# Kernel optimization log

Hardware: AMD Instinct MI355X
Metric: run time of the kernel (lower is better)

## Reference

```python
import jax, jax.numpy as jnp
import numpy as np

ENT_SIZE = 100000; REL_SIZE = 500; ENT_DIM = 256; REL_DIM = 256; H = 256
E = 2048; S = 32; N = 1024; THRESHOLD = 1.0; EPS = 1e-5


def _xav(k, shape):
    fan_in = shape[-1]
    fan_out = shape[-2] if len(shape) > 1 else shape[-1]
    std = (2.0 / (fan_in + fan_out)) ** 0.5
    return jax.random.normal(k, shape, jnp.float32) * std


def setup_inputs() -> dict:
    key = jax.random.key(0)
    ks = jax.random.split(key, 16)
    inp = {}
    inp["neighbors"] = jax.random.randint(ks[0], (E, S), 0, ENT_SIZE)
    inp["pos_h"] = jax.random.randint(ks[1], (N,), 0, E)
    inp["pos_t"] = jax.random.randint(ks[2], (N,), 0, E)
    inp["pos_r"] = jax.random.randint(ks[3], (N,), 0, REL_SIZE)
    inp["neg_h"] = jax.random.randint(ks[4], (N,), 0, E)
    inp["neg_t"] = jax.random.randint(ks[5], (N,), 0, E)
    inp["neg_r"] = jax.random.randint(ks[6], (N,), 0, REL_SIZE)
    inp["ent_embed"] = _xav(ks[7], (ENT_SIZE + 1, ENT_DIM))
    inp["rel_embed"] = _xav(ks[8], (REL_SIZE, REL_DIM))
    inp["trans"] = _xav(ks[9], (2 * REL_SIZE, REL_DIM, ENT_DIM))
    inp["W_ih_f"] = _xav(ks[10], (4 * H, ENT_DIM)); inp["W_hh_f"] = _xav(ks[11], (4 * H, H))
    inp["W_ih_b"] = _xav(ks[12], (4 * H, ENT_DIM)); inp["W_hh_b"] = _xav(ks[13], (4 * H, H))
    inp["b_f"] = jnp.zeros((4 * H,), jnp.float32)
    inp["b_b"] = jnp.zeros((4 * H,), jnp.float32)
    inp["W_lin"] = _xav(ks[14], (ENT_DIM, 2 * H)); inp["b_lin"] = jnp.zeros((ENT_DIM,), jnp.float32)
    inp["gamma"] = jnp.ones((ENT_DIM,), jnp.float32); inp["beta"] = jnp.zeros((ENT_DIM,), jnp.float32)
    return inp


def _lstm_final(x, W_ih, W_hh, b):
    # x: [E,S,D] -> final hidden state [E,H] (PyTorch LSTM gate order i,f,g,o; b = b_ih+b_hh)
    h0 = jnp.zeros((x.shape[0], H), x.dtype)
    def step(carry, xt):
        h, c = carry
        g = xt @ W_ih.T + h @ W_hh.T + b  # [E,4H]
        i, f, gg, o = jnp.split(g, 4, axis=-1)
        c = jax.nn.sigmoid(f) * c + jax.nn.sigmoid(i) * jnp.tanh(gg)
        h = jax.nn.sigmoid(o) * jnp.tanh(c)
        return (h, c), None
    (h, _), _ = jax.lax.scan(step, (h0, h0), jnp.swapaxes(x, 0, 1))
    return h


def _context(ent_embed, neighbors, W_ih_f, W_hh_f, b_f, W_ih_b, W_hh_b, b_b, W_lin, b_lin, gamma, beta):
    x_seq = ent_embed[neighbors]  # [E,S,D]
    h_f = _lstm_final(x_seq, W_ih_f, W_hh_f, b_f)
    h_b = _lstm_final(x_seq[:, ::-1], W_ih_b, W_hh_b, b_b)
    lin = jnp.concatenate([h_f, h_b], -1) @ W_lin.T + b_lin  # [E,ENT_DIM]
    # BatchNorm1d in training mode: batch stats (biased variance)
    mu = lin.mean(0)
    var = lin.var(0)
    return jnp.tanh(gamma * (lin - mu) * jax.lax.rsqrt(var + EPS) + beta)


def _score(trans, rel_embed, ctx, h_idx, r_idx, t_idx):
    Wh = trans[r_idx]             # [N,REL_DIM,ENT_DIM] (grouped expert GEMV, batched)
    Wt = trans[r_idx + REL_SIZE]
    d = jnp.einsum('nre,ne->nr', Wh, ctx[h_idx]) - jnp.einsum('nre,ne->nr', Wt, ctx[t_idx])
    return jnp.linalg.norm(d + rel_embed[r_idx], axis=1)


def reference(neighbors, pos_h, pos_t, pos_r, neg_h, neg_t, neg_r,
              ent_embed, rel_embed, trans, W_ih_f, W_hh_f, W_ih_b, W_hh_b,
              b_f, b_b, W_lin, b_lin, gamma, beta):
    ctx = _context(ent_embed, neighbors, W_ih_f, W_hh_f, b_f, W_ih_b, W_hh_b, b_b,
                   W_lin, b_lin, gamma, beta)
    pos_n = _score(trans, rel_embed, ctx, pos_h, pos_r, pos_t)
    neg_n = _score(trans, rel_embed, ctx, neg_h, neg_r, neg_t)
    return jnp.sum(pos_n + jax.nn.relu(THRESHOLD - neg_n))
```

## Files before the change

### kernel.cpp

```cpp
#include <hip/hip_runtime.h>

constexpr int kE   = 2048;
constexpr int kS   = 32;
constexpr int kD   = 256;
constexpr int kK   = 512;
constexpr int kREL = 500;
constexpr int kN   = 1024;

typedef unsigned short u16;
typedef __attribute__((ext_vector_type(8))) _Float16 f16x8;
typedef __attribute__((ext_vector_type(4))) float    f32x4;
typedef __attribute__((ext_vector_type(4))) unsigned short us4;

static __device__ __forceinline__ u16 f2h(float f) {
  _Float16 h = (_Float16)f;
  return __builtin_bit_cast(u16, h);
}
static __device__ __forceinline__ float h2f(u16 v) {
  _Float16 h = __builtin_bit_cast(_Float16, v);
  return (float)h;
}
static __device__ __forceinline__ float sigf(float x) { return 1.f / (1.f + __expf(-x)); }
static __device__ __forceinline__ float tanhfast(float x) {
  float e = __expf(2.f * x);
  return 1.f - 2.f / (e + 1.f);
}
static __device__ __forceinline__ void gl_lds16(const void* g, void* l) {
  __builtin_amdgcn_global_load_lds((const __attribute__((address_space(1))) unsigned int*)g,
                                   (__attribute__((address_space(3))) unsigned int*)l, 16, 0, 0);
}

__global__ void prep_weights(const float* __restrict__ Wih_f, const float* __restrict__ Whh_f,
                             const float* __restrict__ Wih_b, const float* __restrict__ Whh_b,
                             const float* __restrict__ Wlin_in,
                             u16* __restrict__ Wv3, u16* __restrict__ Whhr,
                             u16* __restrict__ Wlin) {
  int idx = blockIdx.x * 256 + threadIdx.x;
  if (idx < 65536) {
    int q  = idx & 2047;
    int ch = (idx >> 11) & 3;
    int y  = (idx >> 13) & 3;
    int d  = idx >> 15;
    int j  = q >> 3;
    int k8 = (q & 7) ^ (j & 7);
    int jg = y * 256 + j;
    int g = (jg >> 4) & 3, u = (jg >> 6) * 16 + (jg & 15);
    int R = g * 256 + u;
    int k = ch * 64 + k8 * 8;
    const float* src = (d ? Wih_b : Wih_f) + R * 256 + k;
    ushort oa[8];
#pragma unroll
    for (int i = 0; i < 8; i++) oa[i] = f2h(src[i]);
    *(uint4*)((char*)Wv3 + (size_t)idx * 16) = *(uint4*)oa;
  } else if (idx < 131072) {
    int i2 = idx - 65536;
    int d = i2 >> 15;
    int j = (i2 & 32767) >> 5;
    int k = (i2 & 31) * 8;
    int g = (j >> 4) & 3, u = (j >> 6) * 16 + (j & 15);
    int R = g * 256 + u;
    const float* src = (d ? Whh_b : Whh_f) + R * 256 + k;
    ushort oa[8];
#pragma unroll
    for (int i = 0; i < 8; i++) oa[i] = f2h(src[i]);
    *(uint4*)((char*)Whhr + (size_t)i2 * 16) = *(uint4*)oa;
  } else if (idx < 131072 + 16384) {
    int q = (idx - 131072) * 8;
#pragma unroll
    for (int i = 0; i < 8; i++) Wlin[q + i] = f2h(Wlin_in[q + i]);
  }
}

__global__ void gather_x(const int* __restrict__ neighbors, const float* __restrict__ ent,
                         u16* __restrict__ ximg) {
  int idx = blockIdx.x * 256 + threadIdx.x;
  int q    = idx & 511;
  int ch   = (idx >> 9) & 3;
  int tile = (idx >> 11) & 31;
  int s    = idx >> 16;
  int row = q >> 3;
  int c8 = (q & 7) ^ (row & 7);
  int e = tile * 64 + row;
  int k = ch * 64 + c8 * 8;
  int nb = neighbors[e * 32 + s];
  const float* src = ent + (size_t)nb * 256 + k;
  float4 v0 = *(const float4*)src;
  float4 v1 = *(const float4*)(src + 4);
  ushort oa[8];
  oa[0] = f2h(v0.x); oa[1] = f2h(v0.y); oa[2] = f2h(v0.z); oa[3] = f2h(v0.w);
  oa[4] = f2h(v1.x); oa[5] = f2h(v1.y); oa[6] = f2h(v1.z); oa[7] = f2h(v1.w);
  *(uint4*)((char*)ximg + (size_t)idx * 16) = *(uint4*)oa;
}

__global__ __launch_bounds__(256) void xgemm(
    const u16* __restrict__ ximg, const u16* __restrict__ Wv3,
    const float* __restrict__ b_f, const float* __restrict__ b_b,
    u16* __restrict__ gx, int t0, int T) {
  __shared__ __align__(16) char As[8192];
  __shared__ __align__(16) char Bs[32768];
  const int tid = threadIdx.x, lane = tid & 63, w = tid >> 6;
  const int l15 = lane & 15, lq = lane >> 4;
  const int row0 = blockIdx.x * 64;
  const int y = blockIdx.y, dir = blockIdx.z;
  const int tt = row0 >> 11;
  const int e0 = row0 & 2047;
  const int etile = e0 >> 6;
  const int s = dir ? (31 - (t0 + tt)) : (t0 + tt);
  const char* imgA = (const char*)ximg + (size_t)(s * 32 + etile) * 32768;
  const char* imgB = (const char*)Wv3 + (size_t)(dir * 4 + y) * 131072;
  const float* bd = dir ? b_b : b_f;
  const int u = (y * 4 + w) * 16 + l15;

  f32x4 acc[4][4];
#pragma unroll
  for (int n = 0; n < 4; n++) {
    float bv = bd[n * 256 + u];
#pragma unroll
    for (int m = 0; m < 4; m++) acc[m][n] = (f32x4){bv, bv, bv, bv};
  }

  for (int ch = 0; ch < 4; ++ch) {
#pragma unroll
    for (int i = 0; i < 2; i++)
      gl_lds16(imgA + ch * 8192 + i * 4096 + w * 1024 + lane * 16,
               As + i * 4096 + w * 1024);
#pragma unroll
    for (int i = 0; i < 8; i++)
      gl_lds16(imgB + (size_t)ch * 32768 + i * 4096 + w * 1024 + lane * 16,
               Bs + i * 4096 + w * 1024);
    __syncthreads();
#pragma unroll
    for (int ks = 0; ks < 2; ++ks) {
      const int kb = ks * 64 + lq * 16;
      f16x8 a[4], b[4];
#pragma unroll
      for (int m = 0; m < 4; m++) {
        int row = m * 16 + l15;
        a[m] = *(const f16x8*)(As + row * 128 + (kb ^ ((row & 7) << 4)));
      }
#pragma unroll
      for (int n = 0; n < 4; n++) {
        int row = w * 64 + n * 16 + l15;
        b[n] = *(const f16x8*)(Bs + row * 128 + (kb ^ ((row & 7) << 4)));
      }
#pragma unroll
      for (int m = 0; m < 4; m++)
#pragma unroll
        for (int n = 0; n < 4; n++)
          acc[m][n] = __builtin_amdgcn_mfma_f32_16x16x32_f16(a[m], b[n], acc[m][n], 0, 0, 0);
    }
    __syncthreads();
  }

  u16* out = gx + (((size_t)dir * T + tt) * kE) * 1024;
#pragma unroll
  for (int m = 0; m < 4; m++)
#pragma unroll
    for (int r = 0; r < 4; r++) {
      int e = e0 + m * 16 + lq * 4 + r;
      us4 o;
      o[0] = f2h(acc[m][0][r]); o[1] = f2h(acc[m][1][r]);
      o[2] = f2h(acc[m][2][r]); o[3] = f2h(acc[m][3][r]);
      __builtin_nontemporal_store(o, (us4*)(out + ((size_t)e * 256 + u) * 4));
    }
}

__global__ __launch_bounds__(256) void lstm_step(
    const u16* __restrict__ gx, const u16* __restrict__ Whhr,
    const u16* __restrict__ hprev, u16* __restrict__ hnext,
    float* __restrict__ cbuf, int tt, int T) {
  const int tid = threadIdx.x, lane = tid & 63, w = tid >> 6;
  const int l15 = lane & 15, lq = lane >> 4;
  const int bid = blockIdx.x;
  const int dir = bid >> 8;
  const int rem = bid & 255;
  const int jg = rem >> 6;
  const int et = rem & 63;
  const int e0 = et * 32;
  const int c0 = jg * 256 + w * 64;
  const int unit = (c0 >> 6) * 16 + l15;

  const u16* Wd  = Whhr + ((size_t)dir * 1024 + c0) * kD;
  const u16* hpd = hprev + (size_t)dir * kE * kD;
  u16* hnd = hnext + (size_t)dir * kE * kD;
  float* cd = cbuf + (size_t)dir * kE * kD;
  const u16* gp = gx + ((size_t)dir * T + tt) * kE * 1024;

  f32x4 acc[2][4];
#pragma unroll
  for (int m = 0; m < 2; m++)
#pragma unroll
    for (int r = 0; r < 4; r++) {
      us4 g = __builtin_nontemporal_load(
          (const us4*)(gp + (size_t)(e0 + m * 16 + lq * 4 + r) * 1024 + unit * 4));
#pragma unroll
      for (int n = 0; n < 4; n++) acc[m][n][r] = h2f(g[n]);
    }

  const int klane = lq * 8;
#pragma unroll
  for (int ks = 0; ks < 8; ks++) {
    const int ka = ks * 32 + klane;
    f16x8 a[2], b[4];
#pragma unroll
    for (int m = 0; m < 2; m++)
      a[m] = *(const f16x8*)(hpd + (size_t)(e0 + m * 16 + l15) * kD + ka);
#pragma unroll
    for (int n = 0; n < 4; n++)
      b[n] = *(const f16x8*)(Wd + (size_t)(n * 16 + l15) * kD + ka);
#pragma unroll
    for (int m = 0; m < 2; m++)
#pragma unroll
      for (int n = 0; n < 4; n++)
        acc[m][n] = __builtin_amdgcn_mfma_f32_16x16x32_f16(a[m], b[n], acc[m][n], 0, 0, 0);
  }

#pragma unroll
  for (int m = 0; m < 2; m++)
#pragma unroll
    for (int r = 0; r < 4; r++) {
      int row = e0 + m * 16 + lq * 4 + r;
      size_t off = (size_t)row * kD + unit;
      float gi = acc[m][0][r];
      float gf = acc[m][1][r];
      float gg = acc[m][2][r];
      float go = acc[m][3][r];
      float c_old = cd[off];
      float cn = sigf(gf) * c_old + sigf(gi) * tanhfast(gg);
      cd[off] = cn;
      hnd[off] = f2h(sigf(go) * tanhfast(cn));
    }
}

static __device__ __forceinline__ void gemm_tile(
    const u16* __restrict__ Alo, const u16* __restrict__ Ahi,
    const u16* __restrict__ W, int e0,
    u16* As, u16* Bs, f32x4 (&acc)[4][4]) {
  const int tid = threadIdx.x;
  const int lane = tid & 63;
  const int w = tid >> 6;
#pragma unroll
  for (int m = 0; m < 4; m++)
#pragma unroll
    for (int n = 0; n < 4; n++) acc[m][n] = (f32x4){0.f, 0.f, 0.f, 0.f};

  for (int ch = 0; ch < 8; ++ch) {
    const int k0 = ch * 64;
    __syncthreads();
    const u16* Asrc = (k0 < 256) ? Alo : Ahi;
    const int kbase = (k0 < 256) ? k0 : (k0 - 256);
#pragma unroll
    for (int i = 0; i < 2; i++) {
      int idx = tid + i * 256;
      int row = idx >> 3, c8 = idx & 7;
      uint4 v = *(const uint4*)(Asrc + (size_t)(e0 + row) * 256 + kbase + c8 * 8);
      *(uint4*)((char*)As + row * 128 + ((c8 * 16) ^ ((row & 7) << 4))) = v;
    }
#pragma unroll
    for (int i = 0; i < 8; i++) {
      int idx = tid + i * 256;
      int j = idx >> 3, c8 = idx & 7;
      uint4 v = *(const uint4*)(W + (size_t)j * kK + k0 + c8 * 8);
      *(uint4*)((char*)Bs + j * 128 + ((c8 * 16) ^ ((j & 7) << 4))) = v;
    }
    __syncthreads();
#pragma unroll
    for (int ks = 0; ks < 2; ++ks) {
      const int kb = ks * 64 + (lane >> 4) * 16;
      f16x8 a[4], b[4];
#pragma unroll
      for (int m = 0; m < 4; m++) {
        int row = m * 16 + (lane & 15);
        a[m] = *(const f16x8*)((const char*)As + row * 128 + (kb ^ ((row & 7) << 4)));
      }
#pragma unroll
      for (int n = 0; n < 4; n++) {
        int row = w * 64 + n * 16 + (lane & 15);
        b[n] = *(const f16x8*)((const char*)Bs + row * 128 + (kb ^ ((row & 7) << 4)));
      }
#pragma unroll
      for (int m = 0; m < 4; m++)
#pragma unroll
        for (int n = 0; n < 4; n++)
          acc[m][n] = __builtin_amdgcn_mfma_f32_16x16x32_f16(a[m], b[n], acc[m][n], 0, 0, 0);
    }
  }
}

__global__ __launch_bounds__(256) void lin_kernel(
    const u16* __restrict__ hf, const u16* __restrict__ hb,
    const u16* __restrict__ Wl, const float* __restrict__ b_lin,
    float* __restrict__ lin) {
  __shared__ __align__(16) char smem[40960];
  u16* As = (u16*)smem;
  u16* Bs = (u16*)(smem + 8192);
  const int tid = threadIdx.x, lane = tid & 63, w = tid >> 6;
  const int e0 = blockIdx.x * 64;
  f32x4 acc[4][4];
  gemm_tile(hf, hb, Wl, e0, As, Bs, acc);
#pragma unroll
  for (int m = 0; m < 4; m++)
#pragma unroll
    for (int n = 0; n < 4; n++)
#pragma unroll
      for (int r = 0; r < 4; r++) {
        int e = e0 + m * 16 + (lane >> 4) * 4 + r;
        int col = w * 64 + n * 16 + (lane & 15);
        lin[(size_t)e * 256 + col] = acc[m][n][r] + b_lin[col];
      }
}

__global__ void bn_stats(const float* __restrict__ lin, float* __restrict__ part) {
  int b = blockIdx.x, c = threadIdx.x;
  float s = 0.f, s2 = 0.f;
  for (int e = b * 32; e < b * 32 + 32; ++e) {
    float x = lin[(size_t)e * 256 + c];
    s += x; s2 += x * x;
  }
  part[b * 256 + c] = s;
  part[64 * 256 + b * 256 + c] = s2;
}

__global__ void bn_apply(const float* __restrict__ lin, const float* __restrict__ part,
                         const float* __restrict__ gamma, const float* __restrict__ beta,
                         float* __restrict__ ctx) {
  int c = threadIdx.x;
  float s = 0.f, s2 = 0.f;
  for (int b = 0; b < 64; b++) { s += part[b * 256 + c]; s2 += part[64 * 256 + b * 256 + c]; }
  float mu = s * (1.f / 2048.f);
  float rsig = rsqrtf(s2 * (1.f / 2048.f) - mu * mu + 1e-5f);
  float ga = gamma[c], be = beta[c];
  int e0 = blockIdx.x * 8;
  for (int e = e0; e < e0 + 8; ++e) {
    float x = lin[(size_t)e * 256 + c];
    ctx[(size_t)e * 256 + c] = tanhf(ga * (x - mu) * rsig + be);
  }
}

__global__ void group_rel(const int* __restrict__ pr, const int* __restrict__ nr,
                          int* __restrict__ offs, int* __restrict__ list) {
  __shared__ int cnt[512], sc[512], cur[512];
  int tid = threadIdx.x;
  cnt[tid] = 0;
  __syncthreads();
  for (int i = tid; i < 2 * kN; i += 512) {
    int r = (i < kN) ? pr[i] : nr[i - kN];
    atomicAdd(&cnt[r], 1);
  }
  __syncthreads();
  sc[tid] = cnt[tid];
  __syncthreads();
  for (int d = 1; d < 512; d <<= 1) {
    int v = (tid >= d) ? sc[tid - d] : 0;
    __syncthreads();
    sc[tid] += v;
    __syncthreads();
  }
  int excl = (tid == 0) ? 0 : sc[tid - 1];
  cur[tid] = excl;
  if (tid <= kREL) offs[tid] = excl;
  __syncthreads();
  for (int i = tid; i < 2 * kN; i += 512) {
    int r = (i < kN) ? pr[i] : nr[i - kN];
    int p = atomicAdd(&cur[r], 1);
    list[p] = i;
  }
}

__global__ __launch_bounds__(256) void score_grouped(
    const float* __restrict__ ctx, const float* __restrict__ trans,
    const float* __restrict__ rel_embed,
    const int* __restrict__ ph, const int* __restrict__ pt,
    const int* __restrict__ nh, const int* __restrict__ nt,
    const int* __restrict__ offs, const int* __restrict__ list,
    float* __restrict__ scores) {
  int r = blockIdx.x;
  int start = offs[r], end = offs[r + 1];
  if (start >= end) return;
  int tid = threadIdx.x;
  __shared__ float cs[8][2][256];
  __shared__ float red[8][4];
  float relv = rel_embed[r * 256 + tid];
  const float4* Whp = (const float4*)(trans + (size_t)r * 65536 + (size_t)tid * 256);
  const float4* Wtp = (const float4*)(trans + ((size_t)r + kREL) * 65536 + (size_t)tid * 256);

  for (int chunk = start; chunk < end; chunk += 8) {
    int G = min(8, end - chunk);
    for (int j = 0; j < G; j++) {
      int i = list[chunk + j];
      int hh = (i < kN) ? ph[i] : nh[i - kN];
      int tt = (i < kN) ? pt[i] : nt[i - kN];
      cs[j][0][tid] = ctx[(size_t)hh * 256 + tid];
      cs[j][1][tid] = ctx[(size_t)tt * 256 + tid];
    }
    __syncthreads();
    float acc[8];
#pragma unroll
    for (int j = 0; j < 8; j++) acc[j] = relv;
#pragma unroll 2
    for (int q = 0; q < 64; q++) {
      float4 w1 = Whp[q];
      float4 w2 = Wtp[q];
#pragma unroll
      for (int j = 0; j < 8; j++) {
        float4 xh = *(const float4*)&cs[j][0][q * 4];
        float4 xt = *(const float4*)&cs[j][1][q * 4];
        acc[j] += w1.x * xh.x + w1.y * xh.y + w1.z * xh.z + w1.w * xh.w
                - (w2.x * xt.x + w2.y * xt.y + w2.z * xt.z + w2.w * xt.w);
      }
    }
    for (int j = 0; j < G; j++) {
      float sq = acc[j] * acc[j];
      for (int o = 32; o; o >>= 1) sq += __shfl_down(sq, o);
      if ((tid & 63) == 0) red[j][tid >> 6] = sq;
    }
    __syncthreads();
    if (tid < G) {
      float s = red[tid][0] + red[tid][1] + red[tid][2] + red[tid][3];
      scores[list[chunk + tid]] = sqrtf(s);
    }
    __syncthreads();
  }
}

__global__ void final_reduce(const float* __restrict__ scores, float* __restrict__ out) {
  int tid = threadIdx.x;
  float a = 0.f;
  for (int i = tid; i < 2 * kN; i += 256) {
    float s = scores[i];
    a += (i < kN) ? s : fmaxf(0.f, 1.f - s);
  }
  for (int off = 32; off; off >>= 1) a += __shfl_down(a, off);
  __shared__ float w4[4];
  if ((tid & 63) == 0) w4[tid >> 6] = a;
  __syncthreads();
  if (tid == 0) out[0] = w4[0] + w4[1] + w4[2] + w4[3];
}

extern "C" void kernel_launch(void* const* d_in, const int* in_sizes, int n_in,
                              void* d_out, int out_size, void* d_ws, size_t ws_size,
                              hipStream_t stream) {
  const int*   neighbors = (const int*)d_in[0];
  const int*   pos_h = (const int*)d_in[1];
  const int*   pos_t = (const int*)d_in[2];
  const int*   pos_r = (const int*)d_in[3];
  const int*   neg_h = (const int*)d_in[4];
  const int*   neg_t = (const int*)d_in[5];
  const int*   neg_r = (const int*)d_in[6];
  const float* ent_embed = (const float*)d_in[7];
  const float* rel_embed = (const float*)d_in[8];
  const float* trans = (const float*)d_in[9];
  const float* W_ih_f = (const float*)d_in[10];
  const float* W_hh_f = (const float*)d_in[11];
  const float* W_ih_b = (const float*)d_in[12];
  const float* W_hh_b = (const float*)d_in[13];
  const float* b_f = (const float*)d_in[14];
  const float* b_b = (const float*)d_in[15];
  const float* W_lin = (const float*)d_in[16];
  const float* b_lin = (const float*)d_in[17];
  const float* gamma = (const float*)d_in[18];
  const float* beta = (const float*)d_in[19];

  char* ws = (char*)d_ws;
  size_t off = 0;
  auto alloc = [&](size_t bytes) {
    void* p = ws + off;
    off = (off + bytes + 255) & ~(size_t)255;
    return p;
  };
  u16* Wv3    = (u16*)alloc((size_t)65536 * 16);
  u16* Whhr   = (u16*)alloc((size_t)2 * 1024 * kD * 2);
  u16* Wlin   = (u16*)alloc((size_t)256 * kK * 2);
  u16* ximg   = (u16*)alloc((size_t)2097152 * 16);
  u16* h0     = (u16*)alloc((size_t)2 * kE * kD * 2);
  u16* h1     = (u16*)alloc((size_t)2 * kE * kD * 2);
  float* cbuf = (float*)alloc((size_t)2 * kE * kD * 4);
  float* lin  = (float*)alloc((size_t)kE * 256 * 4);
  float* part = (float*)alloc((size_t)2 * 64 * 256 * 4);
  float* ctx  = (float*)alloc((size_t)kE * 256 * 4);
  float* scores = (float*)alloc((size_t)2 * kN * 4);
  int* offsb  = (int*)alloc((size_t)512 * 4);
  int* list   = (int*)alloc((size_t)2 * kN * 4);
  size_t fixed_end = off;
  (void)in_sizes; (void)n_in; (void)out_size;

  int T = 2;
  for (int cand = 32; cand >= 2; cand >>= 1) {
    size_t gxb = (size_t)2 * cand * kE * 1024 * 2;
    if (fixed_end + gxb + (1 << 20) <= ws_size) { T = cand; break; }
  }
  u16* gx = (u16*)alloc((size_t)2 * T * kE * 1024 * 2);

  hipMemsetAsync(h0, 0, (size_t)2 * kE * kD * 2, stream);
  hipMemsetAsync(cbuf, 0, (size_t)2 * kE * kD * 4, stream);

  prep_weights<<<576, 256, 0, stream>>>(W_ih_f, W_hh_f, W_ih_b, W_hh_b, W_lin,
                                        Wv3, Whhr, Wlin);
  gather_x<<<8192, 256, 0, stream>>>(neighbors, ent_embed, ximg);
  group_rel<<<1, 512, 0, stream>>>(pos_r, neg_r, offsb, list);

  for (int t0 = 0; t0 < kS; t0 += T) {
    xgemm<<<dim3(T * 32, 4, 2), 256, 0, stream>>>(ximg, Wv3, b_f, b_b, gx, t0, T);
    for (int tt = 0; tt < T; tt++) {
      int t = t0 + tt;
      const u16* hp = (t & 1) ? h1 : h0;
      u16* hn = (t & 1) ? h0 : h1;
      lstm_step<<<512, 256, 0, stream>>>(gx, Whhr, hp, hn, cbuf, tt, T);
    }
  }

  lin_kernel<<<32, 256, 0, stream>>>(h0, h0 + (size_t)kE * kD, Wlin, b_lin, lin);
  bn_stats<<<64, 256, 0, stream>>>(lin, part);
  bn_apply<<<256, 256, 0, stream>>>(lin, part, gamma, beta, ctx);
  score_grouped<<<kREL, 256, 0, stream>>>(ctx, trans, rel_embed,
                                          pos_h, pos_t, neg_h, neg_t, offsb, list, scores);
  final_reduce<<<1, 256, 0, stream>>>(scores, (float*)d_out);
}
```

Before: 831.4 us.

## Fuse next-step input GEMM into recurrent step kernel with double-buffered gates

Each LSTM step now runs in a single kernel. The first 512 blocks do the recurrent update for step t, and the extra 256 blocks compute the input projection for step t+1 into a ping-pong gate buffer. This replaces the large batched xgemm over many timesteps with per-step overlap and shrinks the gate buffer so it can stay cache-resident, which is why the nontemporal hints are dropped. It also fuses prep_weights with gather_x, and folds the BN partial statistics into lin_kernel to remove bn_stats. The cost is more launches of a heavier kernel, LDS allocated even for recurrent blocks (possibly lowering occupancy), and a shorter xgemm that is less efficient per launch.

```diff
diff --git a/kernel.cpp b/kernel.cpp
--- a/kernel.cpp
+++ b/kernel.cpp
@@ -30,82 +30,77 @@
                                    (__attribute__((address_space(3))) unsigned int*)l, 16, 0, 0);
 }
 
-__global__ void prep_weights(const float* __restrict__ Wih_f, const float* __restrict__ Whh_f,
-                             const float* __restrict__ Wih_b, const float* __restrict__ Whh_b,
-                             const float* __restrict__ Wlin_in,
-                             u16* __restrict__ Wv3, u16* __restrict__ Whhr,
-                             u16* __restrict__ Wlin) {
-  int idx = blockIdx.x * 256 + threadIdx.x;
-  if (idx < 65536) {
-    int q  = idx & 2047;
-    int ch = (idx >> 11) & 3;
-    int y  = (idx >> 13) & 3;
-    int d  = idx >> 15;
-    int j  = q >> 3;
-    int k8 = (q & 7) ^ (j & 7);
-    int jg = y * 256 + j;
-    int g = (jg >> 4) & 3, u = (jg >> 6) * 16 + (jg & 15);
-    int R = g * 256 + u;
-    int k = ch * 64 + k8 * 8;
-    const float* src = (d ? Wih_b : Wih_f) + R * 256 + k;
+__global__ void prep_gather(const float* __restrict__ Wih_f, const float* __restrict__ Whh_f,
+                            const float* __restrict__ Wih_b, const float* __restrict__ Whh_b,
+                            const float* __restrict__ Wlin_in,
+                            const int* __restrict__ neighbors, const float* __restrict__ ent,
+                            u16* __restrict__ Wv3, u16* __restrict__ Whhr,
+                            u16* __restrict__ Wlin, u16* __restrict__ ximg) {
+  if (blockIdx.x < 576) {
+    int idx = blockIdx.x * 256 + threadIdx.x;
+    if (idx < 65536) {
+      int q  = idx & 2047;
+      int ch = (idx >> 11) & 3;
+      int y  = (idx >> 13) & 3;
+      int d  = idx >> 15;
+      int j  = q >> 3;
+      int k8 = (q & 7) ^ (j & 7);
+      int jg = y * 256 + j;
+      int g = (jg >> 4) & 3, u = (jg >> 6) * 16 + (jg & 15);
+      int R = g * 256 + u;
+      int k = ch * 64 + k8 * 8;
+      const float* src = (d ? Wih_b : Wih_f) + R * 256 + k;
+      ushort oa[8];
+#pragma unroll
+      for (int i = 0; i < 8; i++) oa[i] = f2h(src[i]);
+      *(uint4*)((char*)Wv3 + (size_t)idx * 16) = *(uint4*)oa;
+    } else if (idx < 131072) {
+      int i2 = idx - 65536;
+      int d = i2 >> 15;
+      int j = (i2 & 32767) >> 5;
+      int k = (i2 & 31) * 8;
+      int g = (j >> 4) & 3, u = (j >> 6) * 16 + (j & 15);
+      int R = g * 256 + u;
+      const float* src = (d ? Whh_b : Whh_f) + R * 256 + k;
+      ushort oa[8];
+#pragma unroll
+      for (int i = 0; i < 8; i++) oa[i] = f2h(src[i]);
+      *(uint4*)((char*)Whhr + (size_t)i2 * 16) = *(uint4*)oa;
+    } else if (idx < 131072 + 16384) {
+      int q = (idx - 131072) * 8;
+#pragma unroll
+      for (int i = 0; i < 8; i++) Wlin[q + i] = f2h(Wlin_in[q + i]);
+    }
+  } else {
+    int idx = (blockIdx.x - 576) * 256 + threadIdx.x;
+    int q    = idx & 511;
+    int ch   = (idx >> 9) & 3;
+    int tile = (idx >> 11) & 31;
+    int s    = idx >> 16;
+    int row = q >> 3;
+    int c8 = (q & 7) ^ (row & 7);
+    int e = tile * 64 + row;
+    int k = ch * 64 + c8 * 8;
+    int nb = neighbors[e * 32 + s];
+    const float* src = ent + (size_t)nb * 256 + k;
+    float4 v0 = *(const float4*)src;
+    float4 v1 = *(const float4*)(src + 4);
     ushort oa[8];
-#pragma unroll
-    for (int i = 0; i < 8; i++) oa[i] = f2h(src[i]);
-    *(uint4*)((char*)Wv3 + (size_t)idx * 16) = *(uint4*)oa;
-  } else if (idx < 131072) {
-    int i2 = idx - 65536;
-    int d = i2 >> 15;
-    int j = (i2 & 32767) >> 5;
-    int k = (i2 & 31) * 8;
-    int g = (j >> 4) & 3, u = (j >> 6) * 16 + (j & 15);
-    int R = g * 256 + u;
-    const float* src = (d ? Whh_b : Whh_f) + R * 256 + k;
-    ushort oa[8];
-#pragma unroll
-    for (int i = 0; i < 8; i++) oa[i] = f2h(src[i]);
-    *(uint4*)((char*)Whhr + (size_t)i2 * 16) = *(uint4*)oa;
-  } else if (idx < 131072 + 16384) {
-    int q = (idx - 131072) * 8;
-#pragma unroll
-    for (int i = 0; i < 8; i++) Wlin[q + i] = f2h(Wlin_in[q + i]);
-  }
-}
-
-__global__ void gather_x(const int* __restrict__ neighbors, const float* __restrict__ ent,
-                         u16* __restrict__ ximg) {
-  int idx = blockIdx.x * 256 + threadIdx.x;
-  int q    = idx & 511;
-  int ch   = (idx >> 9) & 3;
-  int tile = (idx >> 11) & 31;
-  int s    = idx >> 16;
-  int row = q >> 3;
-  int c8 = (q & 7) ^ (row & 7);
-  int e = tile * 64 + row;
-  int k = ch * 64 + c8 * 8;
-  int nb = neighbors[e * 32 + s];
-  const float* src = ent + (size_t)nb * 256 + k;
-  float4 v0 = *(const float4*)src;
-  float4 v1 = *(const float4*)(src + 4);
-  ushort oa[8];
-  oa[0] = f2h(v0.x); oa[1] = f2h(v0.y); oa[2] = f2h(v0.z); oa[3] = f2h(v0.w);
-  oa[4] = f2h(v1.x); oa[5] = f2h(v1.y); oa[6] = f2h(v1.z); oa[7] = f2h(v1.w);
-  *(uint4*)((char*)ximg + (size_t)idx * 16) = *(uint4*)oa;
-}
-
-__global__ __launch_bounds__(256) void xgemm(
+    oa[0] = f2h(v0.x); oa[1] = f2h(v0.y); oa[2] = f2h(v0.z); oa[3] = f2h(v0.w);
+    oa[4] = f2h(v1.x); oa[5] = f2h(v1.y); oa[6] = f2h(v1.z); oa[7] = f2h(v1.w);
+    *(uint4*)((char*)ximg + (size_t)idx * 16) = *(uint4*)oa;
+  }
+}
+
+static __device__ __forceinline__ void xgemm_body(
     const u16* __restrict__ ximg, const u16* __restrict__ Wv3,
     const float* __restrict__ b_f, const float* __restrict__ b_b,
-    u16* __restrict__ gx, int t0, int T) {
-  __shared__ __align__(16) char As[8192];
-  __shared__ __align__(16) char Bs[32768];
+    u16* __restrict__ gx, int ts, int etile, int y, int dir,
+    char* As, char* Bs) {
   const int tid = threadIdx.x, lane = tid & 63, w = tid >> 6;
   const int l15 = lane & 15, lq = lane >> 4;
-  const int row0 = blockIdx.x * 64;
-  const int y = blockIdx.y, dir = blockIdx.z;
-  const int tt = row0 >> 11;
-  const int e0 = row0 & 2047;
-  const int etile = e0 >> 6;
-  const int s = dir ? (31 - (t0 + tt)) : (t0 + tt);
+  const int e0 = etile * 64;
+  const int s = dir ? (31 - ts) : ts;
   const char* imgA = (const char*)ximg + (size_t)(s * 32 + etile) * 32768;
   const char* imgB = (const char*)Wv3 + (size_t)(dir * 4 + y) * 131072;
   const float* bd = dir ? b_b : b_f;
@@ -152,7 +147,7 @@
     __syncthreads();
   }
 
-  u16* out = gx + (((size_t)dir * T + tt) * kE) * 1024;
+  u16* out = gx + ((size_t)(dir * 2 + (ts & 1)) * kE) * 1024;
 #pragma unroll
   for (int m = 0; m < 4; m++)
 #pragma unroll
@@ -161,17 +156,16 @@
       us4 o;
       o[0] = f2h(acc[m][0][r]); o[1] = f2h(acc[m][1][r]);
       o[2] = f2h(acc[m][2][r]); o[3] = f2h(acc[m][3][r]);
-      __builtin_nontemporal_store(o, (us4*)(out + ((size_t)e * 256 + u) * 4));
-    }
-}
-
-__global__ __launch_bounds__(256) void lstm_step(
+      *(us4*)(out + ((size_t)e * 256 + u) * 4) = o;
+    }
+}
+
+static __device__ __forceinline__ void rec_body(
     const u16* __restrict__ gx, const u16* __restrict__ Whhr,
     const u16* __restrict__ hprev, u16* __restrict__ hnext,
-    float* __restrict__ cbuf, int tt, int T) {
+    float* __restrict__ cbuf, int t, int bid) {
   const int tid = threadIdx.x, lane = tid & 63, w = tid >> 6;
   const int l15 = lane & 15, lq = lane >> 4;
-  const int bid = blockIdx.x;
   const int dir = bid >> 8;
   const int rem = bid & 255;
   const int jg = rem >> 6;
@@ -184,15 +178,14 @@
   const u16* hpd = hprev + (size_t)dir * kE * kD;
   u16* hnd = hnext + (size_t)dir * kE * kD;
   float* cd = cbuf + (size_t)dir * kE * kD;
-  const u16* gp = gx + ((size_t)dir * T + tt) * kE * 1024;
+  const u16* gp = gx + ((size_t)(dir * 2 + (t & 1)) * kE) * 1024;
 
   f32x4 acc[2][4];
 #pragma unroll
   for (int m = 0; m < 2; m++)
 #pragma unroll
     for (int r = 0; r < 4; r++) {
-      us4 g = __builtin_nontemporal_load(
-          (const us4*)(gp + (size_t)(e0 + m * 16 + lq * 4 + r) * 1024 + unit * 4));
+      us4 g = *(const us4*)(gp + (size_t)(e0 + m * 16 + lq * 4 + r) * 1024 + unit * 4);
 #pragma unroll
       for (int n = 0; n < 4; n++) acc[m][n][r] = h2f(g[n]);
     }
@@ -232,6 +225,34 @@
     }
 }
 
+__global__ __launch_bounds__(256) void step_fused(
+    const u16* __restrict__ ximg, const u16* __restrict__ Wv3,
+    const float* __restrict__ b_f, const float* __restrict__ b_b,
+    u16* __restrict__ gx, const u16* __restrict__ Whhr,
+    const u16* __restrict__ hprev, u16* __restrict__ hnext,
+    float* __restrict__ cbuf, int t) {
+  __shared__ __align__(16) char As[8192];
+  __shared__ __align__(16) char Bs[32768];
+  if (blockIdx.x < 512) {
+    rec_body(gx, Whhr, hprev, hnext, cbuf, t, blockIdx.x);
+  } else {
+    int ts = t + 1;
+    if (ts >= kS) return;
+    int b = blockIdx.x - 512;
+    xgemm_body(ximg, Wv3, b_f, b_b, gx, ts, b & 31, (b >> 5) & 3, b >> 7, As, Bs);
+  }
+}
+
+__global__ __launch_bounds__(256) void xgemm_pro(
+    const u16* __restrict__ ximg, const u16* __restrict__ Wv3,
+    const float* __restrict__ b_f, const float* __restrict__ b_b,
+    u16* __restrict__ gx) {
+  __shared__ __align__(16) char As[8192];
+  __shared__ __align__(16) char Bs[32768];
+  int b = blockIdx.x;
+  xgemm_body(ximg, Wv3, b_f, b_b, gx, 0, b & 31, (b >> 5) & 3, b >> 7, As, Bs);
+}
+
 static __device__ __forceinline__ void gemm_tile(
     const u16* __restrict__ Alo, const u16* __restrict__ Ahi,
     const u16* __restrict__ W, int e0,
@@ -290,35 +311,36 @@
 __global__ __launch_bounds__(256) void lin_kernel(
     const u16* __restrict__ hf, const u16* __restrict__ hb,
     const u16* __restrict__ Wl, const float* __restrict__ b_lin,
-    float* __restrict__ lin) {
+    float* __restrict__ lin, float* __restrict__ part) {
   __shared__ __align__(16) char smem[40960];
   u16* As = (u16*)smem;
   u16* Bs = (u16*)(smem + 8192);
   const int tid = threadIdx.x, lane = tid & 63, w = tid >> 6;
+  const int l15 = lane & 15, lq = lane >> 4;
   const int e0 = blockIdx.x * 64;
   f32x4 acc[4][4];
   gemm_tile(hf, hb, Wl, e0, As, Bs, acc);
 #pragma unroll
-  for (int m = 0; m < 4; m++)
-#pragma unroll
-    for (int n = 0; n < 4; n++)
+  for (int n = 0; n < 4; n++) {
+    int col = w * 64 + n * 16 + l15;
+    float bl = b_lin[col];
+    float s1 = 0.f, s2 = 0.f;
+#pragma unroll
+    for (int m = 0; m < 4; m++)
 #pragma unroll
       for (int r = 0; r < 4; r++) {
-        int e = e0 + m * 16 + (lane >> 4) * 4 + r;
-        int col = w * 64 + n * 16 + (lane & 15);
-        lin[(size_t)e * 256 + col] = acc[m][n][r] + b_lin[col];
+        int e = e0 + m * 16 + lq * 4 + r;
+        float v = acc[m][n][r] + bl;
+        lin[(size_t)e * 256 + col] = v;
+        s1 += v; s2 += v * v;
       }
-}
-
-__global__ void bn_stats(const float* __restrict__ lin, float* __restrict__ part) {
-  int b = blockIdx.x, c = threadIdx.x;
-  float s = 0.f, s2 = 0.f;
-  for (int e = b * 32; e < b * 32 + 32; ++e) {
-    float x = lin[(size_t)e * 256 + c];
-    s += x; s2 += x * x;
-  }
-  part[b * 256 + c] = s;
-  part[64 * 256 + b * 256 + c] = s2;
+    s1 += __shfl_down(s1, 16); s2 += __shfl_down(s2, 16);
+    s1 += __shfl_down(s1, 32); s2 += __shfl_down(s2, 32);
+    if (lq == 0) {
+      part[blockIdx.x * 256 + col] = s1;
+      part[8192 + blockIdx.x * 256 + col] = s2;
+    }
+  }
 }
 
 __global__ void bn_apply(const float* __restrict__ lin, const float* __restrict__ part,
@@ -326,7 +348,7 @@
                          float* __restrict__ ctx) {
   int c = threadIdx.x;
   float s = 0.f, s2 = 0.f;
-  for (int b = 0; b < 64; b++) { s += part[b * 256 + c]; s2 += part[64 * 256 + b * 256 + c]; }
+  for (int b = 0; b < 32; b++) { s += part[b * 256 + c]; s2 += part[8192 + b * 256 + c]; }
   float mu = s * (1.f / 2048.f);
   float rsig = rsqrtf(s2 * (1.f / 2048.f) - mu * mu + 1e-5f);
   float ga = gamma[c], be = beta[c];
@@ -475,42 +497,31 @@
   u16* h0     = (u16*)alloc((size_t)2 * kE * kD * 2);
   u16* h1     = (u16*)alloc((size_t)2 * kE * kD * 2);
   float* cbuf = (float*)alloc((size_t)2 * kE * kD * 4);
+  u16* gx     = (u16*)alloc((size_t)2 * 2 * kE * 1024 * 2);
   float* lin  = (float*)alloc((size_t)kE * 256 * 4);
-  float* part = (float*)alloc((size_t)2 * 64 * 256 * 4);
+  float* part = (float*)alloc((size_t)2 * 32 * 256 * 4);
   float* ctx  = (float*)alloc((size_t)kE * 256 * 4);
   float* scores = (float*)alloc((size_t)2 * kN * 4);
   int* offsb  = (int*)alloc((size_t)512 * 4);
   int* list   = (int*)alloc((size_t)2 * kN * 4);
-  size_t fixed_end = off;
-  (void)in_sizes; (void)n_in; (void)out_size;
-
-  int T = 2;
-  for (int cand = 32; cand >= 2; cand >>= 1) {
-    size_t gxb = (size_t)2 * cand * kE * 1024 * 2;
-    if (fixed_end + gxb + (1 << 20) <= ws_size) { T = cand; break; }
-  }
-  u16* gx = (u16*)alloc((size_t)2 * T * kE * 1024 * 2);
+  (void)in_sizes; (void)n_in; (void)out_size; (void)ws_size;
 
   hipMemsetAsync(h0, 0, (size_t)2 * kE * kD * 2, stream);
   hipMemsetAsync(cbuf, 0, (size_t)2 * kE * kD * 4, stream);
 
-  prep_weights<<<576, 256, 0, stream>>>(W_ih_f, W_hh_f, W_ih_b, W_hh_b, W_lin,
-                                        Wv3, Whhr, Wlin);
-  gather_x<<<8192, 256, 0, stream>>>(neighbors, ent_embed, ximg);
+  prep_gather<<<576 + 8192, 256, 0, stream>>>(W_ih_f, W_hh_f, W_ih_b, W_hh_b, W_lin,
+                                              neighbors, ent_embed,
+                                              Wv3, Whhr, Wlin, ximg);
   group_rel<<<1, 512, 0, stream>>>(pos_r, neg_r, offsb, list);
-
-  for (int t0 = 0; t0 < kS; t0 += T) {
-    xgemm<<<dim3(T * 32, 4, 2), 256, 0, stream>>>(ximg, Wv3, b_f, b_b, gx, t0, T);
-    for (int tt = 0; tt < T; tt++) {
-      int t = t0 + tt;
-      const u16* hp = (t & 1) ? h1 : h0;
-      u16* hn = (t & 1) ? h0 : h1;
-      lstm_step<<<512, 256, 0, stream>>>(gx, Whhr, hp, hn, cbuf, tt, T);
-    }
-  }
-
-  lin_kernel<<<32, 256, 0, stream>>>(h0, h0 + (size_t)kE * kD, Wlin, b_lin, lin);
-  bn_stats<<<64, 256, 0, stream>>>(lin, part);
+  xgemm_pro<<<256, 256, 0, stream>>>(ximg, Wv3, b_f, b_b, gx);
+
+  for (int t = 0; t < kS; t++) {
+    const u16* hp = (t & 1) ? h1 : h0;
+    u16* hn = (t & 1) ? h0 : h1;
+    step_fused<<<768, 256, 0, stream>>>(ximg, Wv3, b_f, b_b, gx, Whhr, hp, hn, cbuf, t);
+  }
+
+  lin_kernel<<<32, 256, 0, stream>>>(h0, h0 + (size_t)kE * kD, Wlin, b_lin, lin, part);
   bn_apply<<<256, 256, 0, stream>>>(lin, part, gamma, beta, ctx);
   score_grouped<<<kREL, 256, 0, stream>>>(ctx, trans, rel_embed,
                                           pos_h, pos_t, neg_h, neg_t, offsb, list, scores);
```

Measured after the change: 870.7 us. 1.05x slower.
